# Kernel tuning notes

Hardware: AMD Instinct MI355X
Metric: run time of the kernel (lower is better)

Reference implementation:

```python
import jax, jax.numpy as jnp
import numpy as np

N = 50000    # nodes
E = 800000   # edges (avg degree 16)
H = 4        # attention heads
IN = 128     # input feature size
HID = 128    # hidden size per head
OUT = 64     # output size per head
GAT_SLOPE = 0.2   # DGL GATConv internal LeakyReLU slope
ACT_SLOPE = 0.01  # nn.LeakyReLU default slope


def _lrelu(x, s):
    return jnp.where(x >= 0, x, s * x)


def _gat_conv(x, src, dst, W, attn_l, attn_r, bias, heads, out_dim):
    """DGL GATConv (feat_drop disabled for deterministic reference).
    x: [N, F_in] -> out: [N, heads, out_dim]"""
    z = (x @ W).reshape(N, heads, out_dim)                 # [N,H,D]
    el = jnp.sum(z * attn_l, axis=-1)                      # [N,H]
    er = jnp.sum(z * attn_r, axis=-1)                      # [N,H]
    e = _lrelu(el[src] + er[dst], GAT_SLOPE)               # [E,H]
    # edge softmax over incoming edges of each dst node (numerically stable)
    emax = jax.ops.segment_max(e, dst, num_segments=N)     # [N,H]
    ex = jnp.exp(e - emax[dst])                            # [E,H]
    esum = jax.ops.segment_sum(ex, dst, num_segments=N)    # [N,H]
    alpha = ex / esum[dst]                                 # [E,H]
    msg = alpha[:, :, None] * z[src]                       # [E,H,D]
    out = jax.ops.segment_sum(msg, dst, num_segments=N)    # [N,H,D]
    return out + bias.reshape(1, heads, out_dim)


def setup_inputs() -> dict:
    key = jax.random.key(0)
    ks = jax.random.split(key, 20)
    def nrm(k, shape, scale=0.05):
        return jax.random.normal(k, shape, dtype=jnp.float32) * scale
    return {
        "n_feat": jax.random.normal(ks[0], (N, IN), dtype=jnp.float32),
        "src": jax.random.randint(ks[1], (E,), 0, N),
        "dst": jax.random.randint(ks[2], (E,), 0, N),
        # input GATConv: IN -> HID x H
        "g0_W": nrm(ks[3], (IN, H * HID)),
        "g0_al": nrm(ks[4], (H, HID)),
        "g0_ar": nrm(ks[5], (H, HID)),
        "g0_b": jnp.zeros((H * HID,), jnp.float32),
        "d0_W": nrm(ks[6], (HID, H * HID)),
        "d0_b": jnp.zeros((HID,), jnp.float32),
        # middle GATConv: HID -> HID x H
        "g1_W": nrm(ks[7], (HID, H * HID)),
        "g1_al": nrm(ks[8], (H, HID)),
        "g1_ar": nrm(ks[9], (H, HID)),
        "g1_b": jnp.zeros((H * HID,), jnp.float32),
        "d1_W": nrm(ks[10], (HID, H * HID)),
        "d1_b": jnp.zeros((HID,), jnp.float32),
        # output GATConv: HID -> OUT x H
        "g2_W": nrm(ks[11], (HID, H * OUT)),
        "g2_al": nrm(ks[12], (H, OUT)),
        "g2_ar": nrm(ks[13], (H, OUT)),
        "g2_b": jnp.zeros((H * OUT,), jnp.float32),
    }


def reference(n_feat, src, dst,
              g0_W, g0_al, g0_ar, g0_b, d0_W, d0_b,
              g1_W, g1_al, g1_ar, g1_b, d1_W, d1_b,
              g2_W, g2_al, g2_ar, g2_b):
    # input GAT + dense
    h = _gat_conv(n_feat, src, dst, g0_W, g0_al, g0_ar, g0_b, H, HID)  # [N,H,HID]
    h = _lrelu(h, ACT_SLOPE).reshape(N, H * HID)
    h = _lrelu(h @ d0_W.T + d0_b, ACT_SLOPE)                            # [N,HID]
    # middle GAT + dense
    h = _gat_conv(h, src, dst, g1_W, g1_al, g1_ar, g1_b, H, HID)
    h = _lrelu(h, ACT_SLOPE).reshape(N, H * HID)
    h = _lrelu(h @ d1_W.T + d1_b, ACT_SLOPE)                            # [N,HID]
    # output GAT, mean over heads
    h = _gat_conv(h, src, dst, g2_W, g2_al, g2_ar, g2_b, H, OUT)        # [N,H,OUT]
    h = _lrelu(h, ACT_SLOPE)
    h = jnp.mean(h, axis=-2)                                            # [N,OUT]
    h = _lrelu(h, ACT_SLOPE)
    return h
```

## Files before the change

kernel.cpp:

```cpp
#include <hip/hip_runtime.h>

#define NN 50000
#define EE 800000
#define HH 4

typedef __attribute__((ext_vector_type(8))) short short8v;
typedef __attribute__((ext_vector_type(4))) float f32x4;
typedef __attribute__((ext_vector_type(4))) unsigned short ushort4v;

__device__ __forceinline__ float b2f(unsigned short u) {
    return __uint_as_float(((unsigned int)u) << 16);
}
__device__ __forceinline__ unsigned short f2b(float f) {
    unsigned int x = __float_as_uint(f);
    x += 0x7fffu + ((x >> 16) & 1u);
    return (unsigned short)(x >> 16);
}

template<int WR, bool ACT, int WEL>
__global__ __launch_bounds__(256) void mgemm_k(
    const unsigned short* __restrict__ A, const unsigned short* __restrict__ Bt,
    const float* __restrict__ bias, unsigned short* __restrict__ C,
    const float* __restrict__ al, const float* __restrict__ ar,
    float* __restrict__ el, float* __restrict__ er,
    int M, int N, int K, float slope)
{
    constexpr int BM = 64 * WR;
    constexpr int NA = 2 * WR;
    __shared__ unsigned short smem[BM * 72 + 128 * 72];
    unsigned short* As = smem;
    unsigned short* Bs = smem + BM * 72;
    unsigned short* Cs = smem;
    const int t   = threadIdx.x;
    const int m0  = blockIdx.y * BM;
    const int n0  = blockIdx.x * 128;
    const int w   = t >> 6;
    const int l   = t & 63;
    const int lr  = l & 15;
    const int lk8 = (l >> 4) * 8;
    const int wbase = w * 16 * WR;

    f32x4 acc[WR][8];
    #pragma unroll
    for (int rr = 0; rr < WR; ++rr)
        #pragma unroll
        for (int i = 0; i < 8; ++i) acc[rr][i] = (f32x4)0.f;

    short8v ra[NA], rb[4];
    auto LOAD = [&](int k0) {
        #pragma unroll
        for (int cc = 0; cc < NA; ++cc) {
            int c = t + cc * 256;
            int row = c >> 3, seg = (c & 7) * 8;
            int gm = m0 + row;
            ra[cc] = (short8v)0;
            if (gm < M)
                ra[cc] = *reinterpret_cast<const short8v*>(
                    &A[(size_t)gm * K + k0 + seg]);
        }
        #pragma unroll
        for (int cc = 0; cc < 4; ++cc) {
            int c = t + cc * 256;
            int row = c >> 3, seg = (c & 7) * 8;
            rb[cc] = *reinterpret_cast<const short8v*>(
                &Bt[(size_t)(n0 + row) * K + k0 + seg]);
        }
    };

    LOAD(0);
    for (int k0 = 0; k0 < K; k0 += 64) {
        #pragma unroll
        for (int cc = 0; cc < NA; ++cc) {
            int c = t + cc * 256;
            *reinterpret_cast<short8v*>(&As[(c >> 3) * 72 + (c & 7) * 8]) = ra[cc];
        }
        #pragma unroll
        for (int cc = 0; cc < 4; ++cc) {
            int c = t + cc * 256;
            *reinterpret_cast<short8v*>(&Bs[(c >> 3) * 72 + (c & 7) * 8]) = rb[cc];
        }
        __syncthreads();
        if (k0 + 64 < K) LOAD(k0 + 64);
        #pragma unroll
        for (int kk = 0; kk < 64; kk += 32) {
            short8v a[WR];
            #pragma unroll
            for (int rr = 0; rr < WR; ++rr)
                a[rr] = *reinterpret_cast<const short8v*>(
                    &As[(wbase + rr * 16 + lr) * 72 + kk + lk8]);
            #pragma unroll
            for (int nb = 0; nb < 8; ++nb) {
                short8v b = *reinterpret_cast<const short8v*>(
                    &Bs[(nb * 16 + lr) * 72 + kk + lk8]);
                #pragma unroll
                for (int rr = 0; rr < WR; ++rr)
                    acc[rr][nb] = __builtin_amdgcn_mfma_f32_16x16x32_bf16(
                        a[rr], b, acc[rr][nb], 0, 0, 0);
            }
        }
        __syncthreads();
    }

    if (WEL > 0) {
        const int nbh = (WEL == 1) ? 8 : 4;
        const int Dd  = (WEL == 1) ? 128 : 64;
        #pragma unroll
        for (int hh = 0; hh < WEL; ++hh) {
            int head = (WEL == 1) ? blockIdx.x : blockIdx.x * 2 + hh;
            #pragma unroll
            for (int rr = 0; rr < WR; ++rr) {
                float pl[4] = {}, pr[4] = {};
                #pragma unroll
                for (int nb = 0; nb < nbh; ++nb) {
                    float alv = al[head * Dd + nb * 16 + lr];
                    float arv = ar[head * Dd + nb * 16 + lr];
                    #pragma unroll
                    for (int r = 0; r < 4; ++r) {
                        float z = acc[rr][hh * nbh + nb][r];
                        pl[r] = fmaf(z, alv, pl[r]);
                        pr[r] = fmaf(z, arv, pr[r]);
                    }
                }
                #pragma unroll
                for (int r = 0; r < 4; ++r) {
                    #pragma unroll
                    for (int o = 1; o < 16; o <<= 1) {
                        pl[r] += __shfl_xor(pl[r], o);
                        pr[r] += __shfl_xor(pr[r], o);
                    }
                }
                if (lr == 0) {
                    #pragma unroll
                    for (int r = 0; r < 4; ++r) {
                        int gm = m0 + wbase + rr * 16 + (l >> 4) * 4 + r;
                        if (gm < M) {
                            el[gm * HH + head] = pl[r];
                            er[gm * HH + head] = pr[r];
                        }
                    }
                }
            }
        }
    }

    #pragma unroll
    for (int rr = 0; rr < WR; ++rr) {
        #pragma unroll
        for (int nb = 0; nb < 8; ++nb) {
            #pragma unroll
            for (int r = 0; r < 4; ++r) {
                int row = wbase + rr * 16 + (l >> 4) * 4 + r;
                int gn = n0 + nb * 16 + lr;
                float v = acc[rr][nb][r];
                if (ACT) { v += bias[gn]; v = v >= 0.f ? v : slope * v; }
                Cs[row * 136 + nb * 16 + lr] = f2b(v);
            }
        }
    }
    __syncthreads();
    constexpr int NC = BM / 16;
    #pragma unroll
    for (int cc = 0; cc < NC; ++cc) {
        int c = t + cc * 256;
        int row = c >> 4, seg = (c & 15) * 8;
        int gm = m0 + row;
        if (gm < M) {
            short8v v = *reinterpret_cast<const short8v*>(&Cs[row * 136 + seg]);
            *reinterpret_cast<short8v*>(&C[(size_t)gm * N + n0 + seg]) = v;
        }
    }
}

#define PREP_T 1796608
__global__ __launch_bounds__(256) void prep_k(
    const float* __restrict__ n_feat, const float* __restrict__ d0_W,
    const float* __restrict__ d1_W, const float* __restrict__ g0_W,
    const float* __restrict__ g1_W, const float* __restrict__ g2_W,
    unsigned short* __restrict__ xF, unsigned short* __restrict__ d0t,
    unsigned short* __restrict__ d1t, unsigned short* __restrict__ g0t,
    unsigned short* __restrict__ g1t, unsigned short* __restrict__ g2t)
{
    int i = blockIdx.x * blockDim.x + threadIdx.x;
    if (i >= PREP_T) return;
    if (i < 1632768) {
        const float* src; unsigned short* dstp; int j;
        if (i < 1600000)      { src = n_feat; dstp = xF;  j = i; }
        else if (i < 1616384) { src = d0_W;   dstp = d0t; j = i - 1600000; }
        else                  { src = d1_W;   dstp = d1t; j = i - 1616384; }
        float4 v = reinterpret_cast<const float4*>(src)[j];
        ushort4v u;
        u[0] = f2b(v.x); u[1] = f2b(v.y); u[2] = f2b(v.z); u[3] = f2b(v.w);
        reinterpret_cast<ushort4v*>(dstp)[j] = u;
    } else {
        const float* W; unsigned short* Wt; int j, K = 128;
        if (i < 1698304)      { W = g0_W; Wt = g0t; j = i - 1632768; }
        else if (i < 1763840) { W = g1_W; Wt = g1t; j = i - 1698304; }
        else                  { W = g2_W; Wt = g2t; j = i - 1763840; }
        int N = (i < 1763840) ? 512 : 256;
        int n = j / K, k = j - n * K;
        Wt[j] = f2b(W[(size_t)k * N + n]);
    }
}

__global__ void hist_k(const int* __restrict__ dst, int* __restrict__ cnt)
{
    int i = blockIdx.x * blockDim.x + threadIdx.x;
    if (i < EE / 2) {
        int2 d = reinterpret_cast<const int2*>(dst)[i];
        atomicAdd(&cnt[d.x], 1);
        atomicAdd(&cnt[d.y], 1);
    }
}

#define SCAN_B 196
__global__ __launch_bounds__(256) void scan1_k(const int* __restrict__ cnt,
                                               int* __restrict__ offs,
                                               int* __restrict__ bsum)
{
    __shared__ int sh[256];
    int b = blockIdx.x, t = threadIdx.x, i = b * 256 + t;
    int v = (i < NN) ? cnt[i] : 0;
    sh[t] = v;
    __syncthreads();
    #pragma unroll
    for (int o = 1; o < 256; o <<= 1) {
        int add = (t >= o) ? sh[t - o] : 0;
        __syncthreads();
        sh[t] += add;
        __syncthreads();
    }
    if (i < NN) offs[i] = sh[t] - v;
    if (t == 255) bsum[b] = sh[t];
}

__global__ __launch_bounds__(256) void scan2_k(int* __restrict__ bsum)
{
    __shared__ int sh[256];
    int t = threadIdx.x;
    int v = (t < SCAN_B) ? bsum[t] : 0;
    sh[t] = v;
    __syncthreads();
    #pragma unroll
    for (int o = 1; o < 256; o <<= 1) {
        int add = (t >= o) ? sh[t - o] : 0;
        __syncthreads();
        sh[t] += add;
        __syncthreads();
    }
    if (t < SCAN_B) bsum[t] = sh[t] - v;
}

__global__ __launch_bounds__(256) void scan3_k(int* __restrict__ offs,
                                               const int* __restrict__ bsum)
{
    int b = blockIdx.x, t = threadIdx.x, i = b * 256 + t;
    if (i < NN) offs[i] += bsum[b];
    if (i == NN - 1) offs[NN] = EE;
}

__global__ void scatter_k(const int* __restrict__ src, const int* __restrict__ dst,
                          const int* __restrict__ offs, int* __restrict__ cursor,
                          int* __restrict__ srcs_sorted)
{
    int i = blockIdx.x * blockDim.x + threadIdx.x;
    if (i >= EE) return;
    int d = dst[i];
    int p = offs[d] + atomicAdd(&cursor[d], 1);
    srcs_sorted[p] = src[i];
}

template<int D, bool MEAN>
__global__ __launch_bounds__(256) void agg2_k(
    const unsigned short* __restrict__ zb, const float* __restrict__ el,
    const float* __restrict__ er, const int* __restrict__ offs,
    const int* __restrict__ srcs, const float* __restrict__ bias,
    unsigned short* __restrict__ outb, float* __restrict__ outf)
{
    constexpr int HD  = HH * D;
    constexpr int EPL = HD / 64;
    typedef __attribute__((ext_vector_type(EPL))) unsigned short uvec;
    int n = blockIdx.x * 4 + (threadIdx.x >> 6);
    if (n >= NN) return;
    int lane = threadIdx.x & 63;
    int h = lane >> 4;
    int beg = offs[n];
    int cnt_e = offs[n + 1] - beg;
    float erh = er[n * HH + h];

    float acc[EPL] = {};
    float wsum = 0.f;

    if (cnt_e > 0) {
        auto LD = [&](int idx, uvec& v, float& elv) {
            int e = idx < cnt_e ? idx : cnt_e - 1;
            int s = srcs[beg + e];
            elv = el[s * HH + h];
            v = *reinterpret_cast<const uvec*>(&zb[(size_t)s * HD + lane * EPL]);
        };
        auto PROC = [&](const uvec& v, float elv) {
            float x = elv + erh;
            x = x >= 0.f ? x : 0.2f * x;
            float ex = __expf(x);
            wsum += ex;
            #pragma unroll
            for (int j = 0; j < EPL; ++j)
                acc[j] = fmaf(ex, b2f(v[j]), acc[j]);
        };
        uvec v0, v1, v2, v3;
        float e0, e1, e2, e3;
        LD(0, v0, e0); LD(1, v1, e1); LD(2, v2, e2); LD(3, v3, e3);
        for (int c0 = 0; c0 < cnt_e; c0 += 4) {
            PROC(v0, e0); LD(c0 + 4, v0, e0);
            if (c0 + 1 < cnt_e) { PROC(v1, e1); } LD(c0 + 5, v1, e1);
            if (c0 + 2 < cnt_e) { PROC(v2, e2); } LD(c0 + 6, v2, e2);
            if (c0 + 3 < cnt_e) { PROC(v3, e3); } LD(c0 + 7, v3, e3);
        }
    }
    float inv = wsum > 0.f ? 1.f / wsum : 0.f;

    float vv[EPL];
    #pragma unroll
    for (int j = 0; j < EPL; ++j) {
        float v = acc[j] * inv + bias[h * D + (lane & 15) * EPL + j];
        vv[j] = v >= 0.f ? v : 0.01f * v;
    }

    if (!MEAN) {
        uvec u;
        #pragma unroll
        for (int j = 0; j < EPL; ++j) u[j] = f2b(vv[j]);
        *reinterpret_cast<uvec*>(&outb[(size_t)n * HD + lane * EPL]) = u;
    } else {
        #pragma unroll
        for (int j = 0; j < EPL; ++j) {
            float s = vv[j];
            s += __shfl_xor(s, 16);
            s += __shfl_xor(s, 32);
            s *= 0.25f;
            vv[j] = s >= 0.f ? s : 0.01f * s;
        }
        if (lane < 16) {
            float* op = outf + (size_t)n * D + lane * EPL;
            #pragma unroll
            for (int j = 0; j < EPL; j += 4)
                *reinterpret_cast<float4*>(op + j) =
                    make_float4(vv[j], vv[j + 1], vv[j + 2], vv[j + 3]);
        }
    }
}

extern "C" void kernel_launch(void* const* d_in, const int* in_sizes, int n_in,
                              void* d_out, int out_size, void* d_ws, size_t ws_size,
                              hipStream_t stream)
{
    const float* n_feat = (const float*)d_in[0];
    const int*   src    = (const int*)d_in[1];
    const int*   dst    = (const int*)d_in[2];
    const float* g0_W  = (const float*)d_in[3];
    const float* g0_al = (const float*)d_in[4];
    const float* g0_ar = (const float*)d_in[5];
    const float* g0_b  = (const float*)d_in[6];
    const float* d0_W  = (const float*)d_in[7];
    const float* d0_b  = (const float*)d_in[8];
    const float* g1_W  = (const float*)d_in[9];
    const float* g1_al = (const float*)d_in[10];
    const float* g1_ar = (const float*)d_in[11];
    const float* g1_b  = (const float*)d_in[12];
    const float* d1_W  = (const float*)d_in[13];
    const float* d1_b  = (const float*)d_in[14];
    const float* g2_W  = (const float*)d_in[15];
    const float* g2_al = (const float*)d_in[16];
    const float* g2_ar = (const float*)d_in[17];
    const float* g2_b  = (const float*)d_in[18];

    char* ws = (char*)d_ws;
    size_t off = 0;
    auto alloc = [&](size_t bytes) {
        void* p = ws + off;
        off += (bytes + 255) & ~(size_t)255;
        return p;
    };
    unsigned short* zB   = (unsigned short*)alloc((size_t)NN * 512 * 2);
    unsigned short* hB   = (unsigned short*)alloc((size_t)NN * 512 * 2);
    unsigned short* hC   = (unsigned short*)alloc((size_t)NN * 128 * 2);
    unsigned short* xF   = (unsigned short*)alloc((size_t)NN * 128 * 2);
    unsigned short* g0t  = (unsigned short*)alloc(512 * 128 * 2);
    unsigned short* g1t  = (unsigned short*)alloc(512 * 128 * 2);
    unsigned short* g2t  = (unsigned short*)alloc(256 * 128 * 2);
    unsigned short* d0t  = (unsigned short*)alloc(128 * 512 * 2);
    unsigned short* d1t  = (unsigned short*)alloc(128 * 512 * 2);
    float*          el   = (float*)alloc((size_t)NN * HH * 4);
    float*          er   = (float*)alloc((size_t)NN * HH * 4);
    int*            cnt  = (int*)alloc((size_t)NN * 4);
    int*            curs = (int*)alloc((size_t)NN * 4);
    int*            offs = (int*)alloc((size_t)(NN + 1) * 4);
    int*            srcs = (int*)alloc((size_t)EE * 4);
    int*            bsum = (int*)alloc(256 * 4);

    hipMemsetAsync(cnt, 0, (size_t)NN * 4, stream);
    hipMemsetAsync(curs, 0, (size_t)NN * 4, stream);
    hist_k<<<(EE / 2 + 255) / 256, 256, 0, stream>>>(dst, cnt);
    scan1_k<<<SCAN_B, 256, 0, stream>>>(cnt, offs, bsum);
    scan2_k<<<1, 256, 0, stream>>>(bsum);
    scan3_k<<<SCAN_B, 256, 0, stream>>>(offs, bsum);
    scatter_k<<<(EE + 255) / 256, 256, 0, stream>>>(src, dst, offs, curs, srcs);
    prep_k<<<(PREP_T + 255) / 256, 256, 0, stream>>>(
        n_feat, d0_W, d1_W, g0_W, g1_W, g2_W, xF, d0t, d1t, g0t, g1t, g2t);

    const int MT2  = (NN + 127) / 128;
    const int NODB = (NN + 3) / 4;

    mgemm_k<2, false, 1><<<dim3(4, MT2), 256, 0, stream>>>(
        xF, g0t, nullptr, zB, g0_al, g0_ar, el, er, NN, 512, 128, 0.f);
    agg2_k<128, false><<<NODB, 256, 0, stream>>>(zB, el, er, offs, srcs, g0_b,
                                                 hB, nullptr);
    mgemm_k<2, true, 0><<<dim3(1, MT2), 256, 0, stream>>>(
        hB, d0t, d0_b, hC, nullptr, nullptr, nullptr, nullptr, NN, 128, 512, 0.01f);

    mgemm_k<2, false, 1><<<dim3(4, MT2), 256, 0, stream>>>(
        hC, g1t, nullptr, zB, g1_al, g1_ar, el, er, NN, 512, 128, 0.f);
    agg2_k<128, false><<<NODB, 256, 0, stream>>>(zB, el, er, offs, srcs, g1_b,
                                                 hB, nullptr);
    mgemm_k<2, true, 0><<<dim3(1, MT2), 256, 0, stream>>>(
        hB, d1t, d1_b, hC, nullptr, nullptr, nullptr, nullptr, NN, 128, 512, 0.01f);

    mgemm_k<2, false, 2><<<dim3(2, MT2), 256, 0, stream>>>(
        hC, g2t, nullptr, zB, g2_al, g2_ar, el, er, NN, 256, 128, 0.f);
    agg2_k<64, true><<<NODB, 256, 0, stream>>>(zB, el, er, offs, srcs, g2_b,
                                               nullptr, (float*)d_out);
}
```

Baseline: 529.0 us.

## Add projection GEMM that keeps A tile resident and loops over column groups

Introduces pgemm_k for the K=128 GAT projection GEMMs. Each block loads its 128-row A tile once into registers and iterates over all output column groups, instead of launching one block per column group that reloads A each time. This cuts redundant global reads of A and shrinks the grid, at the cost of less parallelism per launch (391 blocks) and a serialized loop over groups. It also folds the cursor zeroing into scan3_k, removing one memset.

```diff
diff --git a/kernel.cpp b/kernel.cpp
--- a/kernel.cpp
+++ b/kernel.cpp
@@ -17,98 +17,89 @@
     return (unsigned short)(x >> 16);
 }
 
-template<int WR, bool ACT, int WEL>
-__global__ __launch_bounds__(256) void mgemm_k(
+template<int NG, int HPG>
+__global__ __launch_bounds__(256) void pgemm_k(
     const unsigned short* __restrict__ A, const unsigned short* __restrict__ Bt,
-    const float* __restrict__ bias, unsigned short* __restrict__ C,
+    unsigned short* __restrict__ C,
     const float* __restrict__ al, const float* __restrict__ ar,
-    float* __restrict__ el, float* __restrict__ er,
-    int M, int N, int K, float slope)
-{
-    constexpr int BM = 64 * WR;
-    constexpr int NA = 2 * WR;
-    __shared__ unsigned short smem[BM * 72 + 128 * 72];
+    float* __restrict__ el, float* __restrict__ er, int M)
+{
+    constexpr int K = 128, N = NG * 128, LDA = 136;
+    __shared__ unsigned short smem[2 * 128 * LDA];
     unsigned short* As = smem;
-    unsigned short* Bs = smem + BM * 72;
-    unsigned short* Cs = smem;
-    const int t   = threadIdx.x;
-    const int m0  = blockIdx.y * BM;
-    const int n0  = blockIdx.x * 128;
-    const int w   = t >> 6;
-    const int l   = t & 63;
-    const int lr  = l & 15;
-    const int lk8 = (l >> 4) * 8;
-    const int wbase = w * 16 * WR;
-
-    f32x4 acc[WR][8];
-    #pragma unroll
-    for (int rr = 0; rr < WR; ++rr)
-        #pragma unroll
-        for (int i = 0; i < 8; ++i) acc[rr][i] = (f32x4)0.f;
-
-    short8v ra[NA], rb[4];
-    auto LOAD = [&](int k0) {
-        #pragma unroll
-        for (int cc = 0; cc < NA; ++cc) {
-            int c = t + cc * 256;
-            int row = c >> 3, seg = (c & 7) * 8;
-            int gm = m0 + row;
-            ra[cc] = (short8v)0;
-            if (gm < M)
-                ra[cc] = *reinterpret_cast<const short8v*>(
-                    &A[(size_t)gm * K + k0 + seg]);
-        }
-        #pragma unroll
-        for (int cc = 0; cc < 4; ++cc) {
-            int c = t + cc * 256;
-            int row = c >> 3, seg = (c & 7) * 8;
+    unsigned short* Bs = smem + 128 * LDA;
+    const int t  = threadIdx.x;
+    const int m0 = blockIdx.x * 128;
+    const int w  = t >> 6, l = t & 63;
+    const int lr = l & 15, lk8 = (l >> 4) * 8;
+    const int wbase = w * 32;
+
+    #pragma unroll
+    for (int cc = 0; cc < 8; ++cc) {
+        int c = t + cc * 256;
+        int row = c >> 4, seg = (c & 15) * 8;
+        int gm = m0 + row;
+        short8v v = (short8v)0;
+        if (gm < M)
+            v = *reinterpret_cast<const short8v*>(&A[(size_t)gm * K + seg]);
+        *reinterpret_cast<short8v*>(&As[row * LDA + seg]) = v;
+    }
+    __syncthreads();
+    short8v afr[4][2];
+    #pragma unroll
+    for (int kk4 = 0; kk4 < 4; ++kk4)
+        #pragma unroll
+        for (int rr = 0; rr < 2; ++rr)
+            afr[kk4][rr] = *reinterpret_cast<const short8v*>(
+                &As[(wbase + rr * 16 + lr) * LDA + kk4 * 32 + lk8]);
+
+    short8v rb[8];
+    auto LOADB = [&](int g) {
+        #pragma unroll
+        for (int cc = 0; cc < 8; ++cc) {
+            int c = t + cc * 256;
+            int row = c >> 4, seg = (c & 15) * 8;
             rb[cc] = *reinterpret_cast<const short8v*>(
-                &Bt[(size_t)(n0 + row) * K + k0 + seg]);
+                &Bt[(size_t)(g * 128 + row) * K + seg]);
         }
     };
-
-    LOAD(0);
-    for (int k0 = 0; k0 < K; k0 += 64) {
-        #pragma unroll
-        for (int cc = 0; cc < NA; ++cc) {
-            int c = t + cc * 256;
-            *reinterpret_cast<short8v*>(&As[(c >> 3) * 72 + (c & 7) * 8]) = ra[cc];
-        }
-        #pragma unroll
-        for (int cc = 0; cc < 4; ++cc) {
-            int c = t + cc * 256;
-            *reinterpret_cast<short8v*>(&Bs[(c >> 3) * 72 + (c & 7) * 8]) = rb[cc];
-        }
-        __syncthreads();
-        if (k0 + 64 < K) LOAD(k0 + 64);
-        #pragma unroll
-        for (int kk = 0; kk < 64; kk += 32) {
-            short8v a[WR];
-            #pragma unroll
-            for (int rr = 0; rr < WR; ++rr)
-                a[rr] = *reinterpret_cast<const short8v*>(
-                    &As[(wbase + rr * 16 + lr) * 72 + kk + lk8]);
+    LOADB(0);
+
+    for (int g = 0; g < NG; ++g) {
+        __syncthreads();
+        #pragma unroll
+        for (int cc = 0; cc < 8; ++cc) {
+            int c = t + cc * 256;
+            *reinterpret_cast<short8v*>(&Bs[(c >> 4) * LDA + (c & 15) * 8]) = rb[cc];
+        }
+        __syncthreads();
+        if (g + 1 < NG) LOADB(g + 1);
+
+        f32x4 acc[2][8];
+        #pragma unroll
+        for (int rr = 0; rr < 2; ++rr)
+            #pragma unroll
+            for (int nb = 0; nb < 8; ++nb) acc[rr][nb] = (f32x4)0.f;
+        #pragma unroll
+        for (int kk4 = 0; kk4 < 4; ++kk4) {
             #pragma unroll
             for (int nb = 0; nb < 8; ++nb) {
                 short8v b = *reinterpret_cast<const short8v*>(
-                    &Bs[(nb * 16 + lr) * 72 + kk + lk8]);
-                #pragma unroll
-                for (int rr = 0; rr < WR; ++rr)
-                    acc[rr][nb] = __builtin_amdgcn_mfma_f32_16x16x32_bf16(
-                        a[rr], b, acc[rr][nb], 0, 0, 0);
+                    &Bs[(nb * 16 + lr) * LDA + kk4 * 32 + lk8]);
+                acc[0][nb] = __builtin_amdgcn_mfma_f32_16x16x32_bf16(
+                    afr[kk4][0], b, acc[0][nb], 0, 0, 0);
+                acc[1][nb] = __builtin_amdgcn_mfma_f32_16x16x32_bf16(
+                    afr[kk4][1], b, acc[1][nb], 0, 0, 0);
             }
         }
-        __syncthreads();
-    }
-
-    if (WEL > 0) {
-        const int nbh = (WEL == 1) ? 8 : 4;
-        const int Dd  = (WEL == 1) ? 128 : 64;
-        #pragma unroll
-        for (int hh = 0; hh < WEL; ++hh) {
-            int head = (WEL == 1) ? blockIdx.x : blockIdx.x * 2 + hh;
-            #pragma unroll
-            for (int rr = 0; rr < WR; ++rr) {
+
+        constexpr int nbh = 8 / HPG;
+        constexpr int Dd  = (HPG == 1) ? 128 : 64;
+        #pragma unroll
+        for (int hh = 0; hh < HPG; ++hh) {
+            int head = g * HPG + hh;
+            #pragma unroll
+            for (int rr = 0; rr < 2; ++rr) {
                 float pl[4] = {}, pr[4] = {};
                 #pragma unroll
                 for (int nb = 0; nb < nbh; ++nb) {
@@ -141,12 +132,114 @@
                 }
             }
         }
-    }
-
-    #pragma unroll
-    for (int rr = 0; rr < WR; ++rr) {
-        #pragma unroll
-        for (int nb = 0; nb < 8; ++nb) {
+
+        #pragma unroll
+        for (int rr = 0; rr < 2; ++rr)
+            #pragma unroll
+            for (int nb = 0; nb < 8; ++nb)
+                #pragma unroll
+                for (int r = 0; r < 4; ++r) {
+                    int row = wbase + rr * 16 + (l >> 4) * 4 + r;
+                    As[row * LDA + nb * 16 + lr] = f2b(acc[rr][nb][r]);
+                }
+        __syncthreads();
+        #pragma unroll
+        for (int cc = 0; cc < 8; ++cc) {
+            int c = t + cc * 256;
+            int row = c >> 4, seg = (c & 15) * 8;
+            int gm = m0 + row;
+            if (gm < M)
+                *reinterpret_cast<short8v*>(&C[(size_t)gm * N + g * 128 + seg]) =
+                    *reinterpret_cast<const short8v*>(&As[row * LDA + seg]);
+        }
+    }
+}
+
+template<bool ACT>
+__global__ __launch_bounds__(256) void mgemm_k(
+    const unsigned short* __restrict__ A, const unsigned short* __restrict__ Bt,
+    const float* __restrict__ bias, unsigned short* __restrict__ C,
+    int M, int N, int K, float slope)
+{
+    constexpr int BM = 128;
+    __shared__ unsigned short smem[BM * 72 + 128 * 72];
+    unsigned short* As = smem;
+    unsigned short* Bs = smem + BM * 72;
+    unsigned short* Cs = smem;
+    const int t   = threadIdx.x;
+    const int m0  = blockIdx.y * BM;
+    const int n0  = blockIdx.x * 128;
+    const int w   = t >> 6;
+    const int l   = t & 63;
+    const int lr  = l & 15;
+    const int lk8 = (l >> 4) * 8;
+    const int wbase = w * 32;
+
+    f32x4 acc[2][8];
+    #pragma unroll
+    for (int rr = 0; rr < 2; ++rr)
+        #pragma unroll
+        for (int i = 0; i < 8; ++i) acc[rr][i] = (f32x4)0.f;
+
+    short8v ra[4], rb[4];
+    auto LOAD = [&](int k0) {
+        #pragma unroll
+        for (int cc = 0; cc < 4; ++cc) {
+            int c = t + cc * 256;
+            int row = c >> 3, seg = (c & 7) * 8;
+            int gm = m0 + row;
+            ra[cc] = (short8v)0;
+            if (gm < M)
+                ra[cc] = *reinterpret_cast<const short8v*>(
+                    &A[(size_t)gm * K + k0 + seg]);
+        }
+        #pragma unroll
+        for (int cc = 0; cc < 4; ++cc) {
+            int c = t + cc * 256;
+            int row = c >> 3, seg = (c & 7) * 8;
+            rb[cc] = *reinterpret_cast<const short8v*>(
+                &Bt[(size_t)(n0 + row) * K + k0 + seg]);
+        }
+    };
+
+    LOAD(0);
+    for (int k0 = 0; k0 < K; k0 += 64) {
+        #pragma unroll
+        for (int cc = 0; cc < 4; ++cc) {
+            int c = t + cc * 256;
+            *reinterpret_cast<short8v*>(&As[(c >> 3) * 72 + (c & 7) * 8]) = ra[cc];
+        }
+        #pragma unroll
+        for (int cc = 0; cc < 4; ++cc) {
+            int c = t + cc * 256;
+            *reinterpret_cast<short8v*>(&Bs[(c >> 3) * 72 + (c & 7) * 8]) = rb[cc];
+        }
+        __syncthreads();
+        if (k0 + 64 < K) LOAD(k0 + 64);
+        #pragma unroll
+        for (int kk = 0; kk < 64; kk += 32) {
+            short8v a[2];
+            #pragma unroll
+            for (int rr = 0; rr < 2; ++rr)
+                a[rr] = *reinterpret_cast<const short8v*>(
+                    &As[(wbase + rr * 16 + lr) * 72 + kk + lk8]);
+            #pragma unroll
+            for (int nb = 0; nb < 8; ++nb) {
+                short8v b = *reinterpret_cast<const short8v*>(
+                    &Bs[(nb * 16 + lr) * 72 + kk + lk8]);
+                #pragma unroll
+                for (int rr = 0; rr < 2; ++rr)
+                    acc[rr][nb] = __builtin_amdgcn_mfma_f32_16x16x32_bf16(
+                        a[rr], b, acc[rr][nb], 0, 0, 0);
+            }
+        }
+        __syncthreads();
+    }
+
+    #pragma unroll
+    for (int rr = 0; rr < 2; ++rr)
+        #pragma unroll
+        for (int nb = 0; nb < 8; ++nb)
             #pragma unroll
             for (int r = 0; r < 4; ++r) {
                 int row = wbase + rr * 16 + (l >> 4) * 4 + r;
@@ -155,12 +248,9 @@
                 if (ACT) { v += bias[gn]; v = v >= 0.f ? v : slope * v; }
                 Cs[row * 136 + nb * 16 + lr] = f2b(v);
             }
-        }
-    }
     __syncthreads();
-    constexpr int NC = BM / 16;
-    #pragma unroll
-    for (int cc = 0; cc < NC; ++cc) {
+    #pragma unroll
+    for (int cc = 0; cc < 8; ++cc) {
         int c = t + cc * 256;
         int row = c >> 4, seg = (c & 15) * 8;
         int gm = m0 + row;
@@ -251,10 +341,11 @@
 }
 
 __global__ __launch_bounds__(256) void scan3_k(int* __restrict__ offs,
-                                               const int* __restrict__ bsum)
+                                               const int* __restrict__ bsum,
+                                               int* __restrict__ curs)
 {
     int b = blockIdx.x, t = threadIdx.x, i = b * 256 + t;
-    if (i < NN) offs[i] += bsum[b];
+    if (i < NN) { offs[i] += bsum[b]; curs[i] = 0; }
     if (i == NN - 1) offs[NN] = EE;
 }
 
@@ -398,11 +489,10 @@
     int*            bsum = (int*)alloc(256 * 4);
 
     hipMemsetAsync(cnt, 0, (size_t)NN * 4, stream);
-    hipMemsetAsync(curs, 0, (size_t)NN * 4, stream);
     hist_k<<<(EE / 2 + 255) / 256, 256, 0, stream>>>(dst, cnt);
     scan1_k<<<SCAN_B, 256, 0, stream>>>(cnt, offs, bsum);
     scan2_k<<<1, 256, 0, stream>>>(bsum);
-    scan3_k<<<SCAN_B, 256, 0, stream>>>(offs, bsum);
+    scan3_k<<<SCAN_B, 256, 0, stream>>>(offs, bsum, curs);
     scatter_k<<<(EE + 255) / 256, 256, 0, stream>>>(src, dst, offs, curs, srcs);
     prep_k<<<(PREP_T + 255) / 256, 256, 0, stream>>>(
         n_feat, d0_W, d1_W, g0_W, g1_W, g2_W, xF, d0t, d1t, g0t, g1t, g2t);
@@ -410,22 +500,19 @@
     const int MT2  = (NN + 127) / 128;
     const int NODB = (NN + 3) / 4;
 
-    mgemm_k<2, false, 1><<<dim3(4, MT2), 256, 0, stream>>>(
-        xF, g0t, nullptr, zB, g0_al, g0_ar, el, er, NN, 512, 128, 0.f);
+    pgemm_k<4, 1><<<MT2, 256, 0, stream>>>(xF, g0t, zB, g0_al, g0_ar, el, er, NN);
     agg2_k<128, false><<<NODB, 256, 0, stream>>>(zB, el, er, offs, srcs, g0_b,
                                                  hB, nullptr);
-    mgemm_k<2, true, 0><<<dim3(1, MT2), 256, 0, stream>>>(
-        hB, d0t, d0_b, hC, nullptr, nullptr, nullptr, nullptr, NN, 128, 512, 0.01f);
-
-    mgemm_k<2, false, 1><<<dim3(4, MT2), 256, 0, stream>>>(
-        hC, g1t, nullptr, zB, g1_al, g1_ar, el, er, NN, 512, 128, 0.f);
+    mgemm_k<true><<<dim3(1, MT2), 256, 0, stream>>>(
+        hB, d0t, d0_b, hC, NN, 128, 512, 0.01f);
+
+    pgemm_k<4, 1><<<MT2, 256, 0, stream>>>(hC, g1t, zB, g1_al, g1_ar, el, er, NN);
     agg2_k<128, false><<<NODB, 256, 0, stream>>>(zB, el, er, offs, srcs, g1_b,
                                                  hB, nullptr);
-    mgemm_k<2, true, 0><<<dim3(1, MT2), 256, 0, stream>>>(
-        hB, d1t, d1_b, hC, nullptr, nullptr, nullptr, nullptr, NN, 128, 512, 0.01f);
-
-    mgemm_k<2, false, 2><<<dim3(2, MT2), 256, 0, stream>>>(
-        hC, g2t, nullptr, zB, g2_al, g2_ar, el, er, NN, 256, 128, 0.f);
+    mgemm_k<true><<<dim3(1, MT2), 256, 0, stream>>>(
+        hB, d1t, d1_b, hC, NN, 128, 512, 0.01f);
+
+    pgemm_k<2, 2><<<MT2, 256, 0, stream>>>(hC, g2t, zB, g2_al, g2_ar, el, er, NN);
     agg2_k<64, true><<<NODB, 256, 0, stream>>>(zB, el, er, offs, srcs, g2_b,
                                                nullptr, (float*)d_out);
 }
```

Result: slower. 578.8 us (+9.4%).
